# Performance work log

Measured on AMD Instinct MI355X. Metric: run time of the kernel, lower is better.

## Reference

```python
import jax, jax.numpy as jnp
import numpy as np

B, S, L, F = 4, 4, 1024, 256
D, H = 256, 8
DH = D // H


def setup_inputs() -> dict:
    key = jax.random.key(0)
    ks = jax.random.split(key, 9)
    scale = 0.06  # ~1/sqrt(fan_in) init scale
    return {
        "x": jax.random.normal(ks[0], (B, S, L, F), dtype=jnp.float32),
        "Wq": jax.random.normal(ks[1], (D, F), dtype=jnp.float32) * scale,
        "bq": jnp.zeros((D,), dtype=jnp.float32),
        "Wk": jax.random.normal(ks[2], (D, F), dtype=jnp.float32) * scale,
        "bk": jnp.zeros((D,), dtype=jnp.float32),
        "Wv": jax.random.normal(ks[3], (D, F), dtype=jnp.float32) * scale,
        "bv": jnp.zeros((D,), dtype=jnp.float32),
        "Wo": jax.random.normal(ks[4], (D, D), dtype=jnp.float32) * scale,
        "bo": jnp.zeros((D,), dtype=jnp.float32),
    }


def reference(x, Wq, bq, Wk, bk, Wv, bv, Wo, bo):
    b, s, l, f = x.shape
    xr = x.reshape(b * s, l, f)  # [N, L, F] with N = batch*samples

    def split_heads(t):  # [N, L, D] -> [N, H, L, DH]
        return t.reshape(b * s, l, H, DH).transpose(0, 2, 1, 3)

    q = split_heads(xr @ Wq.T + bq)
    k = split_heads(xr @ Wk.T + bk)
    v = split_heads(xr @ Wv.T + bv)

    scores = jnp.einsum("nhqd,nhkd->nhqk", q, k) / jnp.sqrt(jnp.float32(DH))
    probs = jax.nn.softmax(scores, axis=-1)  # [N, H, L, L] — materialized as in original
    out = jnp.einsum("nhqk,nhkd->nhqd", probs, v)

    out = out.transpose(0, 2, 1, 3).reshape(b * s, l, D)
    out = out @ Wo.T + bo
    out = out.reshape(b, s, l, D)

    # softmax pooling over seq_len (dim=2)
    weight = jax.nn.softmax(out, axis=2)
    return jnp.sum(out * weight, axis=2)  # [B, S, D]
```

## Files before the change

### kernel.cpp

```cpp
#include <hip/hip_runtime.h>
#include <math.h>

#define N_SEQ 16
#define LEN   1024
#define FDIM  256
#define DDIM  256
#define NHEAD 8
#define DHD   32
#define ROWS  (N_SEQ * LEN)
#define QSCALE 0.17677669529663687f
#define LOG2E  1.4426950408889634f
#define QKVN  ((size_t)N_SEQ * NHEAD * LEN * DHD)

typedef __attribute__((ext_vector_type(8))) short bf16x8;
typedef __attribute__((ext_vector_type(4))) float f32x4;

__device__ __forceinline__ unsigned short f2bf(float f) {
    unsigned int u = __float_as_uint(f);
    unsigned int r = u + 0x7fffu + ((u >> 16) & 1u);
    return (unsigned short)(r >> 16);
}

#if __has_builtin(__builtin_amdgcn_exp2f)
#define EXP2F(x) __builtin_amdgcn_exp2f(x)
#else
#define EXP2F(x) __expf((x) * 0.6931471805599453f)
#endif

__device__ __forceinline__ unsigned int pack_bf16_trunc(float p0, float p1) {
    return __builtin_amdgcn_perm(__float_as_uint(p1), __float_as_uint(p0), 0x07060302u);
}

__device__ __forceinline__ void load_lds16(const void* g, void* l) {
    __builtin_amdgcn_global_load_lds(
        (const __attribute__((address_space(1))) unsigned int*)g,
        (__attribute__((address_space(3))) unsigned int*)l, 16, 0, 0);
}

__global__ __launch_bounds__(256) void convert_bf16(
    const float* __restrict__ X,
    const float* __restrict__ Wq, const float* __restrict__ Wk,
    const float* __restrict__ Wv, const float* __restrict__ Wo,
    unsigned short* __restrict__ Xbf, unsigned short* __restrict__ Wbf)
{
    const size_t idx4 = ((size_t)blockIdx.x * 256 + threadIdx.x) * 4;
    const float* src;
    unsigned short* dst;
    if (idx4 < (size_t)ROWS * FDIM) {
        src = X + idx4;
        dst = Xbf + idx4;
    } else {
        const size_t wi = idx4 - (size_t)ROWS * FDIM;
        const int w = (int)(wi >> 16);
        const size_t off = wi & 65535;
        const float* Ws[4] = {Wq, Wk, Wv, Wo};
        src = Ws[w] + off;
        dst = Wbf + wi;
    }
    float4 v = *(const float4*)src;
    ushort4 u;
    u.x = f2bf(v.x); u.y = f2bf(v.y); u.z = f2bf(v.z); u.w = f2bf(v.w);
    *(ushort4*)dst = u;
}

template <int MODE>
__global__ __launch_bounds__(256) void gemm_bf16(
    const unsigned short* __restrict__ Ag, const unsigned short* __restrict__ Bg,
    const float* __restrict__ b0, const float* __restrict__ b1,
    const float* __restrict__ b2,
    unsigned short* __restrict__ OutB,
    float* __restrict__ pmO, float* __restrict__ plO, float* __restrict__ psO)
{
    __shared__ unsigned short As[16 * 512];
    __shared__ unsigned short Bs[16 * 512];

    const int tid  = threadIdx.x;
    const int wv   = tid >> 6;
    const int lane = tid & 63;
    const int l15  = lane & 15;
    const int quad = lane >> 4;
    const int wr = (wv & 1) * 64;
    const int wc = (wv >> 1) * 64;

    int mat = 0, cb = 0, abase, bbase;
    const unsigned short* __restrict__ Astage;
    const unsigned short* __restrict__ Bstage;
    if (MODE == 0) {
        mat = blockIdx.y >> 1;
        cb  = (blockIdx.y & 1) * 128;
        if (mat < 2) {
            Astage = Bg + (size_t)mat * 65536; abase = cb;
            Bstage = Ag;                       bbase = blockIdx.x * 128;
        } else {
            Astage = Ag;                       abase = blockIdx.x * 128;
            Bstage = Bg + (size_t)2 * 65536;   bbase = cb;
        }
    } else {
        Astage = Ag; abase = blockIdx.x * 128;
        Bstage = Bg; bbase = blockIdx.y * 128;
    }

    const int isB = wv >> 1;
    const unsigned short* __restrict__ Mg = isB ? Bstage : Astage;
    const int mb0 = isB ? bbase : abase;
    unsigned short* Ms = isB ? Bs : As;
    const int fbase = (wv & 1) * 8;

    f32x4 acc[4][4] = {};

    for (int kt = 0; kt < 4; ++kt) {
        __syncthreads();
        #pragma unroll
        for (int f = 0; f < 8; ++f) {
            const int fi = fbase + f;
            const int i = fi >> 1, ks = fi & 1;
            load_lds16(Mg + (size_t)(mb0 + i*16 + l15) * 256 + kt*64 + ks*32 + quad*8,
                       Ms + fi * 512);
        }
        __syncthreads();
        #pragma unroll
        for (int ks = 0; ks < 2; ++ks) {
            bf16x8 af[4], bfr[4];
            #pragma unroll
            for (int i = 0; i < 4; ++i)
                af[i] = *(const bf16x8*)(&As[((((wv & 1)*4 + i)*2) + ks)*512 + lane*8]);
            #pragma unroll
            for (int j = 0; j < 4; ++j)
                bfr[j] = *(const bf16x8*)(&Bs[((((wv >> 1)*4 + j)*2) + ks)*512 + lane*8]);
            #pragma unroll
            for (int i = 0; i < 4; ++i)
                #pragma unroll
                for (int j = 0; j < 4; ++j)
                    acc[i][j] = __builtin_amdgcn_mfma_f32_16x16x32_bf16(
                        af[i], bfr[j], acc[i][j], 0, 0, 0);
        }
    }

    if (MODE == 0) {
        if (mat < 2) {
            const float scale = (mat == 0) ? QSCALE * LOG2E : 1.0f;
            const float* __restrict__ bias = (mat == 0) ? b0 : b1;
            unsigned short* __restrict__ Out = OutB + (size_t)mat * QKVN;
            #pragma unroll
            for (int i = 0; i < 4; ++i) {
                const int c0 = cb + wr + i*16 + quad*4;
                const int h = c0 >> 5, dh = c0 & 31;
                const float4 bv4 = *(const float4*)(bias + c0);
                #pragma unroll
                for (int j = 0; j < 4; ++j) {
                    const int r = bbase + wc + j*16 + l15;
                    const int n = r >> 10, l = r & 1023;
                    ushort4 u;
                    u.x = f2bf((acc[i][j][0] + bv4.x) * scale);
                    u.y = f2bf((acc[i][j][1] + bv4.y) * scale);
                    u.z = f2bf((acc[i][j][2] + bv4.z) * scale);
                    u.w = f2bf((acc[i][j][3] + bv4.w) * scale);
                    *(ushort4*)(Out + ((size_t)(n*NHEAD + h) * LEN + l) * DHD + dh) = u;
                }
            }
        } else {
            unsigned short* __restrict__ Vf = OutB + 2 * QKVN;
            #pragma unroll
            for (int j = 0; j < 4; ++j) {
                const int cc = cb + wc + j*16 + l15;
                const int h = cc >> 5, dh = cc & 31;
                const int dhb = dh >> 4, mv = dh & 15;
                const float bv = b2[cc];
                #pragma unroll
                for (int i = 0; i < 4; ++i) {
                    const int r0 = abase + wr + i*16 + quad*4;
                    const int n = r0 >> 10, l0 = r0 & 1023;
                    const int nh = n*NHEAD + h;
                    const int kb = l0 >> 5;
                    const int qv = (l0 & 31) >> 3, jv0 = l0 & 7;
                    const size_t addr =
                        (((size_t)nh*32 + kb)*2 + dhb)*512 + (qv*16 + mv)*8 + jv0;
                    ushort4 u;
                    u.x = f2bf(acc[i][j][0] + bv);
                    u.y = f2bf(acc[i][j][1] + bv);
                    u.z = f2bf(acc[i][j][2] + bv);
                    u.w = f2bf(acc[i][j][3] + bv);
                    *(ushort4*)(Vf + addr) = u;
                }
            }
        }
    } else {
        const int n    = blockIdx.x >> 3;
        const int tile = blockIdx.x & 7;
        __shared__ float red[4][64];

        float bv[4];
        #pragma unroll
        for (int j = 0; j < 4; ++j) bv[j] = b0[bbase + wc + j*16 + l15];
        #pragma unroll
        for (int i = 0; i < 4; ++i)
            #pragma unroll
            for (int j = 0; j < 4; ++j)
                #pragma unroll
                for (int rr = 0; rr < 4; ++rr)
                    acc[i][j][rr] += bv[j];

        float M[4];
        #pragma unroll
        for (int j = 0; j < 4; ++j) {
            float m = -1e30f;
            #pragma unroll
            for (int i = 0; i < 4; ++i)
                #pragma unroll
                for (int rr = 0; rr < 4; ++rr) m = fmaxf(m, acc[i][j][rr]);
            m = fmaxf(m, __shfl_xor(m, 16));
            m = fmaxf(m, __shfl_xor(m, 32));
            M[j] = m;
        }
        if (quad == 0) {
            #pragma unroll
            for (int j = 0; j < 4; ++j) red[wv][j*16 + l15] = M[j];
        }
        __syncthreads();
        #pragma unroll
        for (int j = 0; j < 4; ++j)
            M[j] = fmaxf(red[wv][j*16 + l15], red[wv^1][j*16 + l15]);
        __syncthreads();

        float LE[4], SE[4];
        #pragma unroll
        for (int j = 0; j < 4; ++j) {
            float le = 0.f, se = 0.f;
            #pragma unroll
            for (int i = 0; i < 4; ++i)
                #pragma unroll
                for (int rr = 0; rr < 4; ++rr) {
                    const float z = acc[i][j][rr];
                    const float e = __expf(z - M[j]);
                    le += e; se += z * e;
                }
            le += __shfl_xor(le, 16); le += __shfl_xor(le, 32);
            se += __shfl_xor(se, 16); se += __shfl_xor(se, 32);
            LE[j] = le; SE[j] = se;
        }
        if (quad == 0) {
            #pragma unroll
            for (int j = 0; j < 4; ++j) red[wv][j*16 + l15] = LE[j];
        }
        __syncthreads();
        float LEp[4];
        #pragma unroll
        for (int j = 0; j < 4; ++j) LEp[j] = red[wv^1][j*16 + l15];
        __syncthreads();
        if (quad == 0) {
            #pragma unroll
            for (int j = 0; j < 4; ++j) red[wv][j*16 + l15] = SE[j];
        }
        __syncthreads();
        float SEp[4];
        #pragma unroll
        for (int j = 0; j < 4; ++j) SEp[j] = red[wv^1][j*16 + l15];

        if ((wv & 1) == 0 && quad == 0) {
            #pragma unroll
            for (int j = 0; j < 4; ++j) {
                const int c = bbase + wc + j*16 + l15;
                const size_t o = ((size_t)n*8 + tile)*256 + c;
                pmO[o] = M[j];
                plO[o] = LE[j] + LEp[j];
                psO[o] = SE[j] + SEp[j];
            }
        }
    }
}

#define LDPk 72
__global__ __launch_bounds__(256) void attn_mfma(
    const unsigned short* __restrict__ Qg_, const unsigned short* __restrict__ Kg_,
    const unsigned short* __restrict__ Vf_, unsigned short* __restrict__ Aout)
{
    __shared__ unsigned short Pb[4][2][16 * LDPk];

    const int nh = blockIdx.y;
    const int n  = nh >> 3, h = nh & 7;
    const int q0 = blockIdx.x * 256;
    const int tid  = threadIdx.x;
    const int wv   = tid >> 6;
    const int lane = tid & 63;
    const int l15  = lane & 15;
    const int quad = lane >> 4;

    const unsigned short* __restrict__ Qg = Qg_ + (size_t)nh * LEN * DHD;
    const unsigned short* __restrict__ Kg = Kg_ + (size_t)nh * LEN * DHD;
    const unsigned short* __restrict__ Vf = Vf_ + (size_t)nh * 32768;

    bf16x8 qf[4];
    #pragma unroll
    for (int g = 0; g < 4; ++g)
        qf[g] = *(const bf16x8*)(Qg + (size_t)(q0 + wv*64 + g*16 + l15) * DHD + quad*8);

    f32x4 oA[4] = {{0.f,0.f,0.f,0.f},{0.f,0.f,0.f,0.f},{0.f,0.f,0.f,0.f},{0.f,0.f,0.f,0.f}};
    f32x4 oB[4] = {{0.f,0.f,0.f,0.f},{0.f,0.f,0.f,0.f},{0.f,0.f,0.f,0.f},{0.f,0.f,0.f,0.f}};
    float l_acc[4] = {0.f, 0.f, 0.f, 0.f};

    const unsigned short* __restrict__ kbase = Kg + (size_t)l15 * DHD + quad*8;
    const unsigned short* __restrict__ vbase = Vf + lane*8;

    bf16x8 kf[4], vv[4];
    #pragma unroll
    for (int s = 0; s < 4; ++s) kf[s] = *(const bf16x8*)(kbase + (size_t)(s*16) * DHD);
    #pragma unroll
    for (int j = 0; j < 4; ++j) vv[j] = *(const bf16x8*)(vbase + j*512);

    unsigned short* __restrict__ Pw0 = &Pb[wv][0][0];
    unsigned short* __restrict__ Pw1 = &Pb[wv][1][0];

    for (int t = 0; t < 16; ++t) {
        bf16x8 kn[4], vn[4];
        if (t < 15) {
            #pragma unroll
            for (int s = 0; s < 4; ++s)
                kn[s] = *(const bf16x8*)(kbase + (size_t)((t+1)*64 + s*16) * DHD);
            #pragma unroll
            for (int j = 0; j < 4; ++j)
                vn[j] = *(const bf16x8*)(vbase + ((t+1)*4 + j)*512);
        }
        #pragma unroll
        for (int g = 0; g < 4; ++g) {
            unsigned short* __restrict__ Pcur  = (g & 1) ? Pw1 : Pw0;
            unsigned short* __restrict__ Pprev = (g & 1) ? Pw0 : Pw1;
            f32x4 st[4];
            #pragma unroll
            for (int s = 0; s < 4; ++s) {
                f32x4 z = {0.f, 0.f, 0.f, 0.f};
                st[s] = __builtin_amdgcn_mfma_f32_16x16x32_bf16(kf[s], qf[g], z, 0, 0, 0);
            }
            uint2 pk[4];
            float lg = 0.f;
            #pragma unroll
            for (int s = 0; s < 4; ++s) {
                const float p0 = EXP2F(st[s][0]);
                const float p1 = EXP2F(st[s][1]);
                const float p2 = EXP2F(st[s][2]);
                const float p3 = EXP2F(st[s][3]);
                lg += (p0 + p1) + (p2 + p3);
                pk[s].x = pack_bf16_trunc(p0, p1);
                pk[s].y = pack_bf16_trunc(p2, p3);
            }
            l_acc[g] += lg;
            bf16x8 pf0, pf1;
            if (g > 0) {
                pf0 = *(const bf16x8*)(&Pprev[l15*LDPk + 0*32 + quad*8]);
                pf1 = *(const bf16x8*)(&Pprev[l15*LDPk + 1*32 + quad*8]);
            }
            #pragma unroll
            for (int s = 0; s < 4; ++s)
                *(uint2*)(&Pcur[l15*LDPk + s*16 + quad*4]) = pk[s];
            if (g > 0) {
                oA[g-1] = __builtin_amdgcn_mfma_f32_16x16x32_bf16(vv[0], pf0, oA[g-1], 0, 0, 0);
                oB[g-1] = __builtin_amdgcn_mfma_f32_16x16x32_bf16(vv[1], pf0, oB[g-1], 0, 0, 0);
                oA[g-1] = __builtin_amdgcn_mfma_f32_16x16x32_bf16(vv[2], pf1, oA[g-1], 0, 0, 0);
                oB[g-1] = __builtin_amdgcn_mfma_f32_16x16x32_bf16(vv[3], pf1, oB[g-1], 0, 0, 0);
            }
        }
        {
            bf16x8 pf0 = *(const bf16x8*)(&Pw1[l15*LDPk + 0*32 + quad*8]);
            bf16x8 pf1 = *(const bf16x8*)(&Pw1[l15*LDPk + 1*32 + quad*8]);
            oA[3] = __builtin_amdgcn_mfma_f32_16x16x32_bf16(vv[0], pf0, oA[3], 0, 0, 0);
            oB[3] = __builtin_amdgcn_mfma_f32_16x16x32_bf16(vv[1], pf0, oB[3], 0, 0, 0);
            oA[3] = __builtin_amdgcn_mfma_f32_16x16x32_bf16(vv[2], pf1, oA[3], 0, 0, 0);
            oB[3] = __builtin_amdgcn_mfma_f32_16x16x32_bf16(vv[3], pf1, oB[3], 0, 0, 0);
        }
        if (t < 15) {
            #pragma unroll
            for (int s = 0; s < 4; ++s) kf[s] = kn[s];
            #pragma unroll
            for (int j = 0; j < 4; ++j) vv[j] = vn[j];
        }
    }

    float linv[4];
    #pragma unroll
    for (int g = 0; g < 4; ++g) {
        float tsum = l_acc[g];
        tsum += __shfl_xor(tsum, 16);
        tsum += __shfl_xor(tsum, 32);
        linv[g] = 1.f / tsum;
    }

    float* __restrict__ Tw = (float*)&Pb[wv][0][0];
    const int qr = lane >> 2, c8 = (lane & 3) * 8;
    #pragma unroll
    for (int g = 0; g < 4; ++g) {
        #pragma unroll
        for (int r = 0; r < 4; ++r) {
            Tw[l15*36 + quad*4 + r]      = oA[g][r] * linv[g];
            Tw[l15*36 + 16 + quad*4 + r] = oB[g][r] * linv[g];
        }
        float4 r0 = *(const float4*)(&Tw[qr*36 + c8]);
        float4 r1 = *(const float4*)(&Tw[qr*36 + c8 + 4]);
        unsigned short* dst =
            Aout + ((size_t)(n*LEN + q0 + wv*64 + g*16 + qr)) * DDIM + h*DHD + c8;
        ushort4 u0, u1;
        u0.x = f2bf(r0.x); u0.y = f2bf(r0.y); u0.z = f2bf(r0.z); u0.w = f2bf(r0.w);
        u1.x = f2bf(r1.x); u1.y = f2bf(r1.y); u1.z = f2bf(r1.z); u1.w = f2bf(r1.w);
        *(ushort4*)(dst)     = u0;
        *(ushort4*)(dst + 4) = u1;
    }
}

__global__ __launch_bounds__(256) void pool_merge(
    const float* __restrict__ pm, const float* __restrict__ pl,
    const float* __restrict__ ps, float* __restrict__ out)
{
    const int n = blockIdx.x;
    const int d = threadIdx.x;
    float M = -1e30f;
    #pragma unroll
    for (int t = 0; t < 8; ++t) M = fmaxf(M, pm[((size_t)n*8 + t)*256 + d]);
    float L = 0.f, S = 0.f;
    #pragma unroll
    for (int t = 0; t < 8; ++t) {
        const size_t idx = ((size_t)n*8 + t)*256 + d;
        const float w = __expf(pm[idx] - M);
        L += pl[idx] * w;
        S += ps[idx] * w;
    }
    out[n*256 + d] = S / L;
}

extern "C" void kernel_launch(void* const* d_in, const int* in_sizes, int n_in,
                              void* d_out, int out_size, void* d_ws, size_t ws_size,
                              hipStream_t stream)
{
    const float* x  = (const float*)d_in[0];
    const float* Wq = (const float*)d_in[1];
    const float* bq = (const float*)d_in[2];
    const float* Wk = (const float*)d_in[3];
    const float* bk = (const float*)d_in[4];
    const float* Wv = (const float*)d_in[5];
    const float* bv = (const float*)d_in[6];
    const float* Wo = (const float*)d_in[7];
    const float* bo = (const float*)d_in[8];
    float* out = (float*)d_out;

    char* base = (char*)d_ws;
    unsigned short* Xbf  = (unsigned short*)(base);
    unsigned short* Qb   = (unsigned short*)(base +  8388608);
    unsigned short* Vfrag= (unsigned short*)(base + 25165824);
    unsigned short* attnb= (unsigned short*)(base + 41943040);
    unsigned short* Wbf  = (unsigned short*)(base + 50331648);
    float* pm = (float*)(base + 50855936);
    float* pl = (float*)(base + 50987008);
    float* ps = (float*)(base + 51118080);
    const size_t need_bytes = 51249152;
    if (ws_size < need_bytes) return;

    convert_bf16<<<4352, 256, 0, stream>>>(x, Wq, Wk, Wv, Wo, Xbf, Wbf);
    gemm_bf16<0><<<dim3(ROWS/128, 6), 256, 0, stream>>>(
        Xbf, Wbf, bq, bk, bv, Qb, nullptr, nullptr, nullptr);
    attn_mfma<<<dim3(LEN/256, N_SEQ*NHEAD), 256, 0, stream>>>(
        Qb, Qb + QKVN, Vfrag, attnb);
    gemm_bf16<1><<<dim3(ROWS/128, 2), 256, 0, stream>>>(
        attnb, Wbf + (size_t)768*256, bo, nullptr, nullptr, nullptr, pm, pl, ps);
    pool_merge<<<16, 256, 0, stream>>>(pm, pl, ps, out);
}
```

Measured before the change: 139.1 us.

## Fuse fp32-to-bf16 conversion into GEMM loads and halve attention query tile

Removes the separate convert_bf16 pass. The QKV and output GEMMs now read fp32 X and the weights directly and convert them to bf16 in registers before storing to LDS, which drops a full read/write of the activation tensor and one kernel launch. In exchange the GEMM loads become synchronous register loads instead of direct global-to-LDS transfers. The attention kernel handles 128 queries per block instead of 256 (2 query groups per wave), doubling the grid for more parallelism but re-reading K/V twice as often.

```diff
diff --git a/kernel.cpp b/kernel.cpp
--- a/kernel.cpp
+++ b/kernel.cpp
@@ -1,4 +1,5 @@
 #include <hip/hip_runtime.h>
+#include <hip/hip_bf16.h>
 #include <math.h>
 
 #define N_SEQ 16
@@ -21,6 +22,11 @@
     return (unsigned short)(r >> 16);
 }
 
+__device__ __forceinline__ unsigned int pk_rn(float a, float b) {
+    __hip_bfloat162 h = __float22bfloat162_rn(float2{a, b});
+    unsigned int u; __builtin_memcpy(&u, &h, 4); return u;
+}
+
 #if __has_builtin(__builtin_amdgcn_exp2f)
 #define EXP2F(x) __builtin_amdgcn_exp2f(x)
 #else
@@ -37,35 +43,12 @@
         (__attribute__((address_space(3))) unsigned int*)l, 16, 0, 0);
 }
 
-__global__ __launch_bounds__(256) void convert_bf16(
-    const float* __restrict__ X,
-    const float* __restrict__ Wq, const float* __restrict__ Wk,
-    const float* __restrict__ Wv, const float* __restrict__ Wo,
-    unsigned short* __restrict__ Xbf, unsigned short* __restrict__ Wbf)
-{
-    const size_t idx4 = ((size_t)blockIdx.x * 256 + threadIdx.x) * 4;
-    const float* src;
-    unsigned short* dst;
-    if (idx4 < (size_t)ROWS * FDIM) {
-        src = X + idx4;
-        dst = Xbf + idx4;
-    } else {
-        const size_t wi = idx4 - (size_t)ROWS * FDIM;
-        const int w = (int)(wi >> 16);
-        const size_t off = wi & 65535;
-        const float* Ws[4] = {Wq, Wk, Wv, Wo};
-        src = Ws[w] + off;
-        dst = Wbf + wi;
-    }
-    float4 v = *(const float4*)src;
-    ushort4 u;
-    u.x = f2bf(v.x); u.y = f2bf(v.y); u.z = f2bf(v.z); u.w = f2bf(v.w);
-    *(ushort4*)dst = u;
-}
-
 template <int MODE>
 __global__ __launch_bounds__(256) void gemm_bf16(
-    const unsigned short* __restrict__ Ag, const unsigned short* __restrict__ Bg,
+    const float* __restrict__ A32,
+    const unsigned short* __restrict__ Abf,
+    const float* __restrict__ W0, const float* __restrict__ W1,
+    const float* __restrict__ W2,
     const float* __restrict__ b0, const float* __restrict__ b1,
     const float* __restrict__ b2,
     unsigned short* __restrict__ OutB,
@@ -82,26 +65,26 @@
     const int wr = (wv & 1) * 64;
     const int wc = (wv >> 1) * 64;
 
-    int mat = 0, cb = 0, abase, bbase;
-    const unsigned short* __restrict__ Astage;
-    const unsigned short* __restrict__ Bstage;
+    int mat = 0, cb = 0, abase = 0, bbase = 0;
+    const float* __restrict__ Ast32 = nullptr;
+    const float* __restrict__ Bst32 = nullptr;
     if (MODE == 0) {
         mat = blockIdx.y >> 1;
         cb  = (blockIdx.y & 1) * 128;
         if (mat < 2) {
-            Astage = Bg + (size_t)mat * 65536; abase = cb;
-            Bstage = Ag;                       bbase = blockIdx.x * 128;
+            Ast32 = (mat == 0) ? W0 : W1; abase = cb;
+            Bst32 = A32;                  bbase = blockIdx.x * 128;
         } else {
-            Astage = Ag;                       abase = blockIdx.x * 128;
-            Bstage = Bg + (size_t)2 * 65536;   bbase = cb;
+            Ast32 = A32;  abase = blockIdx.x * 128;
+            Bst32 = W2;   bbase = cb;
         }
     } else {
-        Astage = Ag; abase = blockIdx.x * 128;
-        Bstage = Bg; bbase = blockIdx.y * 128;
+        abase = blockIdx.x * 128;
+        Bst32 = W0; bbase = blockIdx.y * 128;
     }
 
     const int isB = wv >> 1;
-    const unsigned short* __restrict__ Mg = isB ? Bstage : Astage;
+    const float* __restrict__ Mg32 = isB ? Bst32 : Ast32;
     const int mb0 = isB ? bbase : abase;
     unsigned short* Ms = isB ? Bs : As;
     const int fbase = (wv & 1) * 8;
@@ -114,8 +97,19 @@
         for (int f = 0; f < 8; ++f) {
             const int fi = fbase + f;
             const int i = fi >> 1, ks = fi & 1;
-            load_lds16(Mg + (size_t)(mb0 + i*16 + l15) * 256 + kt*64 + ks*32 + quad*8,
-                       Ms + fi * 512);
+            if (MODE == 1 && !isB) {
+                load_lds16(Abf + (size_t)(abase + i*16 + l15) * 256 + kt*64 + ks*32 + quad*8,
+                           Ms + fi * 512);
+            } else {
+                const float* src = Mg32 + (size_t)(mb0 + i*16 + l15) * 256
+                                        + kt*64 + ks*32 + quad*8;
+                float4 x0 = *(const float4*)src;
+                float4 x1 = *(const float4*)(src + 4);
+                uint4 o;
+                o.x = pk_rn(x0.x, x0.y); o.y = pk_rn(x0.z, x0.w);
+                o.z = pk_rn(x1.x, x1.y); o.w = pk_rn(x1.z, x1.w);
+                *(uint4*)(Ms + fi * 512 + lane * 8) = o;
+            }
         }
         __syncthreads();
         #pragma unroll
@@ -278,7 +272,7 @@
 
     const int nh = blockIdx.y;
     const int n  = nh >> 3, h = nh & 7;
-    const int q0 = blockIdx.x * 256;
+    const int q0 = blockIdx.x * 128;
     const int tid  = threadIdx.x;
     const int wv   = tid >> 6;
     const int lane = tid & 63;
@@ -289,14 +283,14 @@
     const unsigned short* __restrict__ Kg = Kg_ + (size_t)nh * LEN * DHD;
     const unsigned short* __restrict__ Vf = Vf_ + (size_t)nh * 32768;
 
-    bf16x8 qf[4];
-    #pragma unroll
-    for (int g = 0; g < 4; ++g)
-        qf[g] = *(const bf16x8*)(Qg + (size_t)(q0 + wv*64 + g*16 + l15) * DHD + quad*8);
-
-    f32x4 oA[4] = {{0.f,0.f,0.f,0.f},{0.f,0.f,0.f,0.f},{0.f,0.f,0.f,0.f},{0.f,0.f,0.f,0.f}};
-    f32x4 oB[4] = {{0.f,0.f,0.f,0.f},{0.f,0.f,0.f,0.f},{0.f,0.f,0.f,0.f},{0.f,0.f,0.f,0.f}};
-    float l_acc[4] = {0.f, 0.f, 0.f, 0.f};
+    bf16x8 qf[2];
+    #pragma unroll
+    for (int g = 0; g < 2; ++g)
+        qf[g] = *(const bf16x8*)(Qg + (size_t)(q0 + wv*32 + g*16 + l15) * DHD + quad*8);
+
+    f32x4 oA[2] = {{0.f,0.f,0.f,0.f},{0.f,0.f,0.f,0.f}};
+    f32x4 oB[2] = {{0.f,0.f,0.f,0.f},{0.f,0.f,0.f,0.f}};
+    float l_acc[2] = {0.f, 0.f};
 
     const unsigned short* __restrict__ kbase = Kg + (size_t)l15 * DHD + quad*8;
     const unsigned short* __restrict__ vbase = Vf + lane*8;
@@ -320,15 +314,34 @@
             for (int j = 0; j < 4; ++j)
                 vn[j] = *(const bf16x8*)(vbase + ((t+1)*4 + j)*512);
         }
-        #pragma unroll
-        for (int g = 0; g < 4; ++g) {
-            unsigned short* __restrict__ Pcur  = (g & 1) ? Pw1 : Pw0;
-            unsigned short* __restrict__ Pprev = (g & 1) ? Pw0 : Pw1;
+        {
             f32x4 st[4];
             #pragma unroll
             for (int s = 0; s < 4; ++s) {
                 f32x4 z = {0.f, 0.f, 0.f, 0.f};
-                st[s] = __builtin_amdgcn_mfma_f32_16x16x32_bf16(kf[s], qf[g], z, 0, 0, 0);
+                st[s] = __builtin_amdgcn_mfma_f32_16x16x32_bf16(kf[s], qf[0], z, 0, 0, 0);
+            }
+            float lg = 0.f;
+            #pragma unroll
+            for (int s = 0; s < 4; ++s) {
+                const float p0 = EXP2F(st[s][0]);
+                const float p1 = EXP2F(st[s][1]);
+                const float p2 = EXP2F(st[s][2]);
+                const float p3 = EXP2F(st[s][3]);
+                lg += (p0 + p1) + (p2 + p3);
+                uint2 pk;
+                pk.x = pack_bf16_trunc(p0, p1);
+                pk.y = pack_bf16_trunc(p2, p3);
+                *(uint2*)(&Pw0[l15*LDPk + s*16 + quad*4]) = pk;
+            }
+            l_acc[0] += lg;
+        }
+        {
+            f32x4 st[4];
+            #pragma unroll
+            for (int s = 0; s < 4; ++s) {
+                f32x4 z = {0.f, 0.f, 0.f, 0.f};
+                st[s] = __builtin_amdgcn_mfma_f32_16x16x32_bf16(kf[s], qf[1], z, 0, 0, 0);
             }
             uint2 pk[4];
             float lg = 0.f;
@@ -342,29 +355,24 @@
                 pk[s].x = pack_bf16_trunc(p0, p1);
                 pk[s].y = pack_bf16_trunc(p2, p3);
             }
-            l_acc[g] += lg;
-            bf16x8 pf0, pf1;
-            if (g > 0) {
-                pf0 = *(const bf16x8*)(&Pprev[l15*LDPk + 0*32 + quad*8]);
-                pf1 = *(const bf16x8*)(&Pprev[l15*LDPk + 1*32 + quad*8]);
-            }
+            l_acc[1] += lg;
+            bf16x8 pf0 = *(const bf16x8*)(&Pw0[l15*LDPk + 0*32 + quad*8]);
+            bf16x8 pf1 = *(const bf16x8*)(&Pw0[l15*LDPk + 1*32 + quad*8]);
             #pragma unroll
             for (int s = 0; s < 4; ++s)
-                *(uint2*)(&Pcur[l15*LDPk + s*16 + quad*4]) = pk[s];
-            if (g > 0) {
-                oA[g-1] = __builtin_amdgcn_mfma_f32_16x16x32_bf16(vv[0], pf0, oA[g-1], 0, 0, 0);
-                oB[g-1] = __builtin_amdgcn_mfma_f32_16x16x32_bf16(vv[1], pf0, oB[g-1], 0, 0, 0);
-                oA[g-1] = __builtin_amdgcn_mfma_f32_16x16x32_bf16(vv[2], pf1, oA[g-1], 0, 0, 0);
-                oB[g-1] = __builtin_amdgcn_mfma_f32_16x16x32_bf16(vv[3], pf1, oB[g-1], 0, 0, 0);
-            }
+                *(uint2*)(&Pw1[l15*LDPk + s*16 + quad*4]) = pk[s];
+            oA[0] = __builtin_amdgcn_mfma_f32_16x16x32_bf16(vv[0], pf0, oA[0], 0, 0, 0);
+            oB[0] = __builtin_amdgcn_mfma_f32_16x16x32_bf16(vv[1], pf0, oB[0], 0, 0, 0);
+            oA[0] = __builtin_amdgcn_mfma_f32_16x16x32_bf16(vv[2], pf1, oA[0], 0, 0, 0);
+            oB[0] = __builtin_amdgcn_mfma_f32_16x16x32_bf16(vv[3], pf1, oB[0], 0, 0, 0);
         }
         {
             bf16x8 pf0 = *(const bf16x8*)(&Pw1[l15*LDPk + 0*32 + quad*8]);
             bf16x8 pf1 = *(const bf16x8*)(&Pw1[l15*LDPk + 1*32 + quad*8]);
-            oA[3] = __builtin_amdgcn_mfma_f32_16x16x32_bf16(vv[0], pf0, oA[3], 0, 0, 0);
-            oB[3] = __builtin_amdgcn_mfma_f32_16x16x32_bf16(vv[1], pf0, oB[3], 0, 0, 0);
-            oA[3] = __builtin_amdgcn_mfma_f32_16x16x32_bf16(vv[2], pf1, oA[3], 0, 0, 0);
-            oB[3] = __builtin_amdgcn_mfma_f32_16x16x32_bf16(vv[3], pf1, oB[3], 0, 0, 0);
+            oA[1] = __builtin_amdgcn_mfma_f32_16x16x32_bf16(vv[0], pf0, oA[1], 0, 0, 0);
+            oB[1] = __builtin_amdgcn_mfma_f32_16x16x32_bf16(vv[1], pf0, oB[1], 0, 0, 0);
+            oA[1] = __builtin_amdgcn_mfma_f32_16x16x32_bf16(vv[2], pf1, oA[1], 0, 0, 0);
+            oB[1] = __builtin_amdgcn_mfma_f32_16x16x32_bf16(vv[3], pf1, oB[1], 0, 0, 0);
         }
         if (t < 15) {
             #pragma unroll
@@ -374,9 +382,9 @@
         }
     }
 
-    float linv[4];
-    #pragma unroll
-    for (int g = 0; g < 4; ++g) {
+    float linv[2];
+    #pragma unroll
+    for (int g = 0; g < 2; ++g) {
         float tsum = l_acc[g];
         tsum += __shfl_xor(tsum, 16);
         tsum += __shfl_xor(tsum, 32);
@@ -386,7 +394,7 @@
     float* __restrict__ Tw = (float*)&Pb[wv][0][0];
     const int qr = lane >> 2, c8 = (lane & 3) * 8;
     #pragma unroll
-    for (int g = 0; g < 4; ++g) {
+    for (int g = 0; g < 2; ++g) {
         #pragma unroll
         for (int r = 0; r < 4; ++r) {
             Tw[l15*36 + quad*4 + r]      = oA[g][r] * linv[g];
@@ -395,7 +403,7 @@
         float4 r0 = *(const float4*)(&Tw[qr*36 + c8]);
         float4 r1 = *(const float4*)(&Tw[qr*36 + c8 + 4]);
         unsigned short* dst =
-            Aout + ((size_t)(n*LEN + q0 + wv*64 + g*16 + qr)) * DDIM + h*DHD + c8;
+            Aout + ((size_t)(n*LEN + q0 + wv*32 + g*16 + qr)) * DDIM + h*DHD + c8;
         ushort4 u0, u1;
         u0.x = f2bf(r0.x); u0.y = f2bf(r0.y); u0.z = f2bf(r0.z); u0.w = f2bf(r0.w);
         u1.x = f2bf(r1.x); u1.y = f2bf(r1.y); u1.z = f2bf(r1.z); u1.w = f2bf(r1.w);
@@ -440,23 +448,20 @@
     float* out = (float*)d_out;
 
     char* base = (char*)d_ws;
-    unsigned short* Xbf  = (unsigned short*)(base);
-    unsigned short* Qb   = (unsigned short*)(base +  8388608);
-    unsigned short* Vfrag= (unsigned short*)(base + 25165824);
-    unsigned short* attnb= (unsigned short*)(base + 41943040);
-    unsigned short* Wbf  = (unsigned short*)(base + 50331648);
-    float* pm = (float*)(base + 50855936);
-    float* pl = (float*)(base + 50987008);
-    float* ps = (float*)(base + 51118080);
-    const size_t need_bytes = 51249152;
+    unsigned short* Qb   = (unsigned short*)(base);
+    unsigned short* attnb= (unsigned short*)(base + 25165824);
+    float* pm = (float*)(base + 33554432);
+    float* pl = (float*)(base + 33685504);
+    float* ps = (float*)(base + 33816576);
+    const size_t need_bytes = 33947648;
     if (ws_size < need_bytes) return;
 
-    convert_bf16<<<4352, 256, 0, stream>>>(x, Wq, Wk, Wv, Wo, Xbf, Wbf);
     gemm_bf16<0><<<dim3(ROWS/128, 6), 256, 0, stream>>>(
-        Xbf, Wbf, bq, bk, bv, Qb, nullptr, nullptr, nullptr);
-    attn_mfma<<<dim3(LEN/256, N_SEQ*NHEAD), 256, 0, stream>>>(
-        Qb, Qb + QKVN, Vfrag, attnb);
+        x, nullptr, Wq, Wk, Wv, bq, bk, bv, Qb, nullptr, nullptr, nullptr);
+    attn_mfma<<<dim3(LEN/128, N_SEQ*NHEAD), 256, 0, stream>>>(
+        Qb, Qb + QKVN, Qb + 2*QKVN, attnb);
     gemm_bf16<1><<<dim3(ROWS/128, 2), 256, 0, stream>>>(
-        attnb, Wbf + (size_t)768*256, bo, nullptr, nullptr, nullptr, pm, pl, ps);
+        nullptr, attnb, Wo, nullptr, nullptr, bo, nullptr, nullptr,
+        nullptr, pm, pl, ps);
     pool_merge<<<16, 256, 0, stream>>>(pm, pl, ps, out);
 }
```

Result: slower. 159.9 us (+15.0%).
